# Kernel optimization log

Measured on AMD Instinct MI355X. Metric: run time of the kernel, lower is better.

Reference implementation:

```python
import jax, jax.numpy as jnp
import numpy as np


def setup_inputs() -> dict:
    key = jax.random.key(0)
    k1, k2 = jax.random.split(key)
    B, N, M, D = 8, 8192, 8192, 3
    gts = jax.random.normal(k1, (B, N, D), dtype=jnp.float32)
    preds = jax.random.normal(k2, (B, M, D), dtype=jnp.float32)
    return {"gts": gts, "preds": preds}


def reference(gts, preds):
    # Chamfer distance (pytorch3d defaults): squared L2, mean over points,
    # mean over batch, sum of both directions.
    x2 = jnp.sum(gts * gts, axis=-1)          # [B, N]
    y2 = jnp.sum(preds * preds, axis=-1)      # [B, M]
    xy = jnp.einsum('bnd,bmd->bnm', gts, preds)  # [B, N, M]
    d2 = x2[:, :, None] + y2[:, None, :] - 2.0 * xy
    d2 = jnp.maximum(d2, 0.0)  # guard tiny negative values from cancellation
    cham_x = jnp.mean(jnp.min(d2, axis=2))  # x -> nearest y, mean over N then B
    cham_y = jnp.mean(jnp.min(d2, axis=1))  # y -> nearest x, mean over M then B
    return cham_x + cham_y
```

## Files before the change

kernel.cpp:

```cpp
#include <hip/hip_runtime.h>
#include <hip/hip_bf16.h>
#include <math.h>


#define BLOCK 256
#define WAVES 4
#define QPW 64
#define NCHUNK 4

typedef short short8 __attribute__((ext_vector_type(8)));
typedef float f32x16 __attribute__((ext_vector_type(16)));

union U16S { uint4 v; short8 s; };

__device__ __forceinline__ unsigned int bf16hi(float f) {
    __hip_bfloat16 h = __float2bfloat16(f);
    return (unsigned int)*reinterpret_cast<unsigned short*>(&h);
}
__device__ __forceinline__ float bf16f(unsigned int u) {
    unsigned short us = (unsigned short)u;
    __hip_bfloat16 h;
    *reinterpret_cast<unsigned short*>(&h) = us;
    return __bfloat162float(h);
}
__device__ __forceinline__ unsigned int encodeKey(float f) {
    unsigned int u = __float_as_uint(f);
    return (u & 0x80000000u) ? ~u : (u | 0x80000000u);
}
__device__ __forceinline__ float decodeKey(unsigned int u) {
    u = (u & 0x80000000u) ? (u & 0x7FFFFFFFu) : ~u;
    return __uint_as_float(u);
}

__device__ __forceinline__ f32x16 mfma_bf16(short8 a, short8 b, f32x16 c) {
    f32x16 d;
    asm volatile("v_mfma_f32_32x32x16_bf16 %0, %1, %2, %3"
                 : "=v"(d) : "v"(a), "v"(b), "v"(c));
    return d;
}
__device__ __forceinline__ void mfma_fence4(f32x16& a, f32x16& b, f32x16& c, f32x16& d) {
    asm volatile("s_nop 7\n\ts_nop 7" : "+v"(a), "+v"(b), "+v"(c), "+v"(d));
}

__global__ void prep_kernel(const float* __restrict__ gts, const float* __restrict__ preds,
                            int nG, int nP, uint4* __restrict__ recG, uint4* __restrict__ recP,
                            unsigned int* __restrict__ keyAll, float* out) {
    const int idx = blockIdx.x * blockDim.x + threadIdx.x;
    if (idx == 0) out[0] = 0.0f;
    if (idx >= nG + nP) return;
    keyAll[idx] = 0u;
    const float* src;
    uint4* dst;
    if (idx < nG) { src = gts + 3 * (size_t)idx;          dst = recG + idx; }
    else          { src = preds + 3 * (size_t)(idx - nG); dst = recP + (idx - nG); }
    const float x = src[0], y = src[1], z = src[2];
    const float w = -0.5f * (x * x + y * y + z * z);
    const unsigned int xh = bf16hi(x), yh = bf16hi(y), zh = bf16hi(z), wh = bf16hi(w);
    const unsigned int xl = bf16hi(x - bf16f(xh));
    const unsigned int yl = bf16hi(y - bf16f(yh));
    const unsigned int zl = bf16hi(z - bf16f(zh));
    const unsigned int wl = bf16hi(w - bf16f(wh));
    *dst = make_uint4(xh | (yh << 16), zh | (wh << 16),
                      xl | (yl << 16), zl | (wl << 16));
}

__global__ void __launch_bounds__(BLOCK, 3)
nn_kernel(const uint4* __restrict__ recG, const uint4* __restrict__ recP,
          unsigned int* __restrict__ keyX, unsigned int* __restrict__ keyY,
          int N, int M, int B) {
    const int z = blockIdx.z;
    const bool dirX = (z < B);
    const int b = dirX ? z : z - B;
    const int NQ = dirX ? N : M;
    const int NR = dirX ? M : N;
    const uint4* Qr = (dirX ? recG : recP) + (size_t)b * NQ;
    const uint4* Rr = (dirX ? recP : recG) + (size_t)b * NR;
    unsigned int* keys = (dirX ? keyX : keyY) + (size_t)b * NQ;

    const int tid = threadIdx.x;
    const int lane = tid & 63;
    const int wave = tid >> 6;
    const int m = lane & 31;
    const bool hiK = lane >= 32;
    const int qBase = (blockIdx.x * WAVES + wave) * QPW;

    const uint4 q0 = Qr[qBase + m];
    const uint4 q1 = Qr[qBase + 32 + m];
    U16S a;
    a.v.x = q0.x;
    a.v.y = (q0.y & 0xFFFFu) | 0x3F800000u;
    a.v.z = hiK ? 0u : q0.z;
    a.v.w = hiK ? 0u : (q0.w & 0xFFFFu);
    const short8 A0 = a.s;
    a.v.x = q1.x;
    a.v.y = (q1.y & 0xFFFFu) | 0x3F800000u;
    a.v.z = hiK ? 0u : q1.z;
    a.v.w = hiK ? 0u : (q1.w & 0xFFFFu);
    const short8 A1 = a.s;

    f32x16 zc;
    #pragma unroll
    for (int r = 0; r < 16; ++r) zc[r] = 0.0f;
    f32x16 k0, k1;
    #pragma unroll
    for (int r = 0; r < 16; ++r) { k0[r] = -INFINITY; k1[r] = -INFINITY; }

    const int chunk = NR / NCHUNK;
    const uint2* rp = (const uint2*)(Rr + (size_t)blockIdx.y * chunk) + 2 * m + (hiK ? 1 : 0);
    const int iters = chunk / 64;

    uint2 t0 = rp[0], t1 = rp[64];
    const uint2* p = rp;
    for (int it = 0; it < iters; ++it) {
        const uint2* pn = (it + 1 < iters) ? (p + 128) : rp;
        const uint2 n0 = pn[0];
        const uint2 n1 = pn[64];

        U16S b0, b1;
        b0.v.x = t0.x; b0.v.y = t0.y;
        b0.v.z = hiK ? 0u : t0.x; b0.v.w = hiK ? 0u : t0.y;
        b1.v.x = t1.x; b1.v.y = t1.y;
        b1.v.z = hiK ? 0u : t1.x; b1.v.w = hiK ? 0u : t1.y;

        f32x16 c0 = mfma_bf16(A0, b0.s, zc);
        f32x16 c1 = mfma_bf16(A1, b0.s, zc);
        f32x16 c2 = mfma_bf16(A0, b1.s, zc);
        f32x16 c3 = mfma_bf16(A1, b1.s, zc);
        mfma_fence4(c0, c1, c2, c3);
        #pragma unroll
        for (int r = 0; r < 16; ++r) {
            k0[r] = fmaxf(fmaxf(c0[r], c2[r]), k0[r]);
            k1[r] = fmaxf(fmaxf(c1[r], c3[r]), k1[r]);
        }

        p = pn; t0 = n0; t1 = n1;
    }

    #pragma unroll
    for (int r = 0; r < 16; ++r) {
        float v0 = k0[r], v1 = k1[r];
        #pragma unroll
        for (int off = 16; off; off >>= 1) {
            v0 = fmaxf(v0, __shfl_xor(v0, off));
            v1 = fmaxf(v1, __shfl_xor(v1, off));
        }
        if (m == 0) {
            const int row = (r & 3) + 8 * (r >> 2) + 4 * (lane >> 5);
            atomicMax(&keys[qBase + row], encodeKey(v0));
            atomicMax(&keys[qBase + 32 + row], encodeKey(v1));
        }
    }
}

__global__ void __launch_bounds__(BLOCK)
reduce_kernel(const unsigned int* __restrict__ keyX, const float* __restrict__ gts, int nG,
              const unsigned int* __restrict__ keyY, const float* __restrict__ preds, int nP,
              float invx, float invy, float* __restrict__ out) {
    const int total = nG + nP;
    float local = 0.0f;
    for (int idx = blockIdx.x * blockDim.x + threadIdx.x; idx < total;
         idx += gridDim.x * blockDim.x) {
        if (idx < nG) {
            const float c = decodeKey(keyX[idx]);
            const float* q = gts + 3 * (size_t)idx;
            const float x2 = q[0] * q[0] + q[1] * q[1] + q[2] * q[2];
            local += fmaxf(x2 - 2.0f * c, 0.0f) * invx;
        } else {
            const int j = idx - nG;
            const float c = decodeKey(keyY[j]);
            const float* q = preds + 3 * (size_t)j;
            const float y2 = q[0] * q[0] + q[1] * q[1] + q[2] * q[2];
            local += fmaxf(y2 - 2.0f * c, 0.0f) * invy;
        }
    }
    __shared__ float waveSums[BLOCK / 64];
    float v = local;
    #pragma unroll
    for (int off = 32; off; off >>= 1) v += __shfl_xor(v, off);
    if ((threadIdx.x & 63) == 0) waveSums[threadIdx.x >> 6] = v;
    __syncthreads();
    if (threadIdx.x == 0) {
        float s = 0.0f;
        #pragma unroll
        for (int w = 0; w < BLOCK / 64; ++w) s += waveSums[w];
        atomicAdd(out, s);
    }
}

extern "C" void kernel_launch(void* const* d_in, const int* in_sizes, int n_in,
                              void* d_out, int out_size, void* d_ws, size_t ws_size,
                              hipStream_t stream) {
    const float* gts   = (const float*)d_in[0];
    const float* preds = (const float*)d_in[1];
    float* out = (float*)d_out;

    const int B = 8;
    const int N = in_sizes[0] / (B * 3);
    const int M = in_sizes[1] / (B * 3);
    const int nG = B * N, nP = B * M;

    uint4* recG = (uint4*)d_ws;
    uint4* recP = recG + nG;
    unsigned int* keyX = (unsigned int*)(recP + nP);
    unsigned int* keyY = keyX + nG;

    prep_kernel<<<(nG + nP + BLOCK - 1) / BLOCK, BLOCK, 0, stream>>>(
        gts, preds, nG, nP, recG, recP, keyX, out);

    dim3 grid(N / (WAVES * QPW), NCHUNK, 2 * B);
    nn_kernel<<<grid, BLOCK, 0, stream>>>(recG, recP, keyX, keyY, N, M, B);

    reduce_kernel<<<(nG + nP + BLOCK - 1) / BLOCK, BLOCK, 0, stream>>>(
        keyX, gts, nG, keyY, preds, nP, 1.0f / (float)nG, 1.0f / (float)nP, out);
}
```

Baseline: 114.6 us.

## Replace atomicMax key reduction with per-chunk partial min buffers and LDS transpose

Drops the encoded-key atomicMax reduction and the key zeroing. Each block now writes per-query partial maxima, found through an LDS transpose, into a buffer per reference chunk, and the reduce kernel combines the two chunks. The reference split drops from 4 chunks to 2, occupancy hint rises to 4, and select-based masking becomes AND masks. The intent is to cut atomic traffic, shuffle reductions and launch bookkeeping. The cost is fewer blocks for parallelism and a prefetch that reads past the chunk end on the last iteration.

New measurement: 98.76 us. 1.16x faster.

```diff
diff --git a/kernel.cpp b/kernel.cpp
--- a/kernel.cpp
+++ b/kernel.cpp
@@ -6,7 +6,7 @@
 #define BLOCK 256
 #define WAVES 4
 #define QPW 64
-#define NCHUNK 4
+#define NCHUNK 2
 
 typedef short short8 __attribute__((ext_vector_type(8)));
 typedef float f32x16 __attribute__((ext_vector_type(16)));
@@ -23,14 +23,6 @@
     *reinterpret_cast<unsigned short*>(&h) = us;
     return __bfloat162float(h);
 }
-__device__ __forceinline__ unsigned int encodeKey(float f) {
-    unsigned int u = __float_as_uint(f);
-    return (u & 0x80000000u) ? ~u : (u | 0x80000000u);
-}
-__device__ __forceinline__ float decodeKey(unsigned int u) {
-    u = (u & 0x80000000u) ? (u & 0x7FFFFFFFu) : ~u;
-    return __uint_as_float(u);
-}
 
 __device__ __forceinline__ f32x16 mfma_bf16(short8 a, short8 b, f32x16 c) {
     f32x16 d;
@@ -44,11 +36,10 @@
 
 __global__ void prep_kernel(const float* __restrict__ gts, const float* __restrict__ preds,
                             int nG, int nP, uint4* __restrict__ recG, uint4* __restrict__ recP,
-                            unsigned int* __restrict__ keyAll, float* out) {
+                            float* out) {
     const int idx = blockIdx.x * blockDim.x + threadIdx.x;
     if (idx == 0) out[0] = 0.0f;
     if (idx >= nG + nP) return;
-    keyAll[idx] = 0u;
     const float* src;
     uint4* dst;
     if (idx < nG) { src = gts + 3 * (size_t)idx;          dst = recG + idx; }
@@ -64,10 +55,9 @@
                       xl | (yl << 16), zl | (wl << 16));
 }
 
-__global__ void __launch_bounds__(BLOCK, 3)
+__global__ void __launch_bounds__(BLOCK, 4)
 nn_kernel(const uint4* __restrict__ recG, const uint4* __restrict__ recP,
-          unsigned int* __restrict__ keyX, unsigned int* __restrict__ keyY,
-          int N, int M, int B) {
+          float* __restrict__ kpart, int N, int M, int B) {
     const int z = blockIdx.z;
     const bool dirX = (z < B);
     const int b = dirX ? z : z - B;
@@ -75,13 +65,15 @@
     const int NR = dirX ? M : N;
     const uint4* Qr = (dirX ? recG : recP) + (size_t)b * NQ;
     const uint4* Rr = (dirX ? recP : recG) + (size_t)b * NR;
-    unsigned int* keys = (dirX ? keyX : keyY) + (size_t)b * NQ;
+    const int nGP = B * (N + M) / 2 * 2;
+    float* outK = kpart + (size_t)blockIdx.y * nGP + (dirX ? 0 : B * N) + (size_t)b * NQ;
 
     const int tid = threadIdx.x;
     const int lane = tid & 63;
     const int wave = tid >> 6;
     const int m = lane & 31;
     const bool hiK = lane >= 32;
+    const unsigned int loMask = hiK ? 0u : 0xFFFFFFFFu;
     const int qBase = (blockIdx.x * WAVES + wave) * QPW;
 
     const uint4 q0 = Qr[qBase + m];
@@ -89,13 +81,13 @@
     U16S a;
     a.v.x = q0.x;
     a.v.y = (q0.y & 0xFFFFu) | 0x3F800000u;
-    a.v.z = hiK ? 0u : q0.z;
-    a.v.w = hiK ? 0u : (q0.w & 0xFFFFu);
+    a.v.z = q0.z & loMask;
+    a.v.w = q0.w & 0xFFFFu & loMask;
     const short8 A0 = a.s;
     a.v.x = q1.x;
     a.v.y = (q1.y & 0xFFFFu) | 0x3F800000u;
-    a.v.z = hiK ? 0u : q1.z;
-    a.v.w = hiK ? 0u : (q1.w & 0xFFFFu);
+    a.v.z = q1.z & loMask;
+    a.v.w = q1.w & 0xFFFFu & loMask;
     const short8 A1 = a.s;
 
     f32x16 zc;
@@ -106,21 +98,20 @@
     for (int r = 0; r < 16; ++r) { k0[r] = -INFINITY; k1[r] = -INFINITY; }
 
     const int chunk = NR / NCHUNK;
-    const uint2* rp = (const uint2*)(Rr + (size_t)blockIdx.y * chunk) + 2 * m + (hiK ? 1 : 0);
+    const uint2* p = (const uint2*)(Rr + (size_t)blockIdx.y * chunk) + 2 * m + (hiK ? 1 : 0);
     const int iters = chunk / 64;
 
-    uint2 t0 = rp[0], t1 = rp[64];
-    const uint2* p = rp;
+    uint2 t0 = p[0], t1 = p[64];
+    #pragma unroll 1
     for (int it = 0; it < iters; ++it) {
-        const uint2* pn = (it + 1 < iters) ? (p + 128) : rp;
-        const uint2 n0 = pn[0];
-        const uint2 n1 = pn[64];
+        const uint2 n0 = p[128];
+        const uint2 n1 = p[192];
 
         U16S b0, b1;
-        b0.v.x = t0.x; b0.v.y = t0.y;
-        b0.v.z = hiK ? 0u : t0.x; b0.v.w = hiK ? 0u : t0.y;
-        b1.v.x = t1.x; b1.v.y = t1.y;
-        b1.v.z = hiK ? 0u : t1.x; b1.v.w = hiK ? 0u : t1.y;
+        b0.v.x = t0.x;          b0.v.y = t0.y;
+        b0.v.z = t0.x & loMask; b0.v.w = t0.y & loMask;
+        b1.v.x = t1.x;          b1.v.y = t1.y;
+        b1.v.z = t1.x & loMask; b1.v.w = t1.y & loMask;
 
         f32x16 c0 = mfma_bf16(A0, b0.s, zc);
         f32x16 c1 = mfma_bf16(A1, b0.s, zc);
@@ -133,45 +124,44 @@
             k1[r] = fmaxf(fmaxf(c1[r], c3[r]), k1[r]);
         }
 
-        p = pn; t0 = n0; t1 = n1;
-    }
-
+        t0 = n0; t1 = n1;
+        p += 128;
+    }
+
+    __shared__ float sT[WAVES][64][36];
     #pragma unroll
     for (int r = 0; r < 16; ++r) {
-        float v0 = k0[r], v1 = k1[r];
-        #pragma unroll
-        for (int off = 16; off; off >>= 1) {
-            v0 = fmaxf(v0, __shfl_xor(v0, off));
-            v1 = fmaxf(v1, __shfl_xor(v1, off));
-        }
-        if (m == 0) {
-            const int row = (r & 3) + 8 * (r >> 2) + 4 * (lane >> 5);
-            atomicMax(&keys[qBase + row], encodeKey(v0));
-            atomicMax(&keys[qBase + 32 + row], encodeKey(v1));
-        }
-    }
+        const int row = (r & 3) + 8 * (r >> 2) + 4 * (lane >> 5);
+        sT[wave][row][m]      = k0[r];
+        sT[wave][32 + row][m] = k1[r];
+    }
+    const float4* rowp = (const float4*)&sT[wave][lane][0];
+    float4 m01 = rowp[0];
+    #pragma unroll
+    for (int kk = 1; kk < 8; ++kk) {
+        const float4 t = rowp[kk];
+        m01.x = fmaxf(m01.x, t.x); m01.y = fmaxf(m01.y, t.y);
+        m01.z = fmaxf(m01.z, t.z); m01.w = fmaxf(m01.w, t.w);
+    }
+    const float cmax = fmaxf(fmaxf(m01.x, m01.y), fmaxf(m01.z, m01.w));
+    outK[qBase + lane] = cmax;
 }
 
 __global__ void __launch_bounds__(BLOCK)
-reduce_kernel(const unsigned int* __restrict__ keyX, const float* __restrict__ gts, int nG,
-              const unsigned int* __restrict__ keyY, const float* __restrict__ preds, int nP,
+reduce_kernel(const float* __restrict__ kpart, const float* __restrict__ gts, int nG,
+              const float* __restrict__ preds, int nP,
               float invx, float invy, float* __restrict__ out) {
     const int total = nG + nP;
     float local = 0.0f;
     for (int idx = blockIdx.x * blockDim.x + threadIdx.x; idx < total;
          idx += gridDim.x * blockDim.x) {
-        if (idx < nG) {
-            const float c = decodeKey(keyX[idx]);
-            const float* q = gts + 3 * (size_t)idx;
-            const float x2 = q[0] * q[0] + q[1] * q[1] + q[2] * q[2];
-            local += fmaxf(x2 - 2.0f * c, 0.0f) * invx;
-        } else {
-            const int j = idx - nG;
-            const float c = decodeKey(keyY[j]);
-            const float* q = preds + 3 * (size_t)j;
-            const float y2 = q[0] * q[0] + q[1] * q[1] + q[2] * q[2];
-            local += fmaxf(y2 - 2.0f * c, 0.0f) * invy;
-        }
+        const float c = fmaxf(kpart[idx], kpart[total + idx]);
+        const float* q;
+        float inv;
+        if (idx < nG) { q = gts + 3 * (size_t)idx;          inv = invx; }
+        else          { q = preds + 3 * (size_t)(idx - nG); inv = invy; }
+        const float q2 = q[0] * q[0] + q[1] * q[1] + q[2] * q[2];
+        local += fmaxf(q2 - 2.0f * c, 0.0f) * inv;
     }
     __shared__ float waveSums[BLOCK / 64];
     float v = local;
@@ -199,17 +189,16 @@
     const int M = in_sizes[1] / (B * 3);
     const int nG = B * N, nP = B * M;
 
-    uint4* recG = (uint4*)d_ws;
-    uint4* recP = recG + nG;
-    unsigned int* keyX = (unsigned int*)(recP + nP);
-    unsigned int* keyY = keyX + nG;
+    uint4* recG  = (uint4*)d_ws;
+    uint4* recP  = recG + nG;
+    float* kpart = (float*)(recP + nP);
 
     prep_kernel<<<(nG + nP + BLOCK - 1) / BLOCK, BLOCK, 0, stream>>>(
-        gts, preds, nG, nP, recG, recP, keyX, out);
+        gts, preds, nG, nP, recG, recP, out);
 
     dim3 grid(N / (WAVES * QPW), NCHUNK, 2 * B);
-    nn_kernel<<<grid, BLOCK, 0, stream>>>(recG, recP, keyX, keyY, N, M, B);
-
-    reduce_kernel<<<(nG + nP + BLOCK - 1) / BLOCK, BLOCK, 0, stream>>>(
-        keyX, gts, nG, keyY, preds, nP, 1.0f / (float)nG, 1.0f / (float)nP, out);
-}
+    nn_kernel<<<grid, BLOCK, 0, stream>>>(recG, recP, kpart, N, M, B);
+
+    reduce_kernel<<<256, BLOCK, 0, stream>>>(
+        kpart, gts, nG, preds, nP, 1.0f / (float)nG, 1.0f / (float)nP, out);
+}
```
